# Kernel optimization log

Measured on AMD Instinct MI355X. Metric: run time of the kernel, lower is better.

The kernel has to match this reference:

```python
import jax, jax.numpy as jnp
import numpy as np

B, H, S, D = 65536, 512, 256, 64  # batch, hidden_dim, memory_slots, slot_size


def setup_inputs() -> dict:
    key = jax.random.key(0)
    ks = jax.random.split(key, 8)
    scale = 1.0 / np.sqrt(H)
    return {
        "query": jax.random.normal(ks[0], (B, H), jnp.float32),
        "content": jax.random.normal(ks[1], (B, H), jnp.float32),
        "memory": jax.random.normal(ks[2], (S, D), jnp.float32),
        "memory_age": jax.random.uniform(ks[3], (S,), jnp.float32, 0.0, 30.0),
        "W_read": jax.random.normal(ks[4], (H, S), jnp.float32) * scale,
        "b_read": jnp.zeros((S,), jnp.float32),
        "W_write": jax.random.normal(ks[5], (H, S), jnp.float32) * scale,
        "b_write": jnp.zeros((S,), jnp.float32),
        "W_content": jax.random.normal(ks[6], (H, D), jnp.float32) * scale,
        "b_content": jnp.zeros((D,), jnp.float32),
    }


def reference(query, content, memory, memory_age,
              W_read, b_read, W_write, b_write, W_content, b_content):
    # ---- read: attention-based addressing over memory slots ----
    read_weights = jax.nn.softmax(query @ W_read + b_read, axis=-1)      # [B, S]
    read_content = read_weights @ memory                                  # [B, D]

    # ---- write: consolidation dynamics (vectorized per-slot EMA) ----
    write_weights = jax.nn.softmax(query @ W_write + b_write, axis=-1)   # [B, S]
    processed_content = content @ W_content + b_content                   # [B, D]
    w_mean = write_weights.mean(axis=0)                                    # [S]
    c_mean = processed_content.mean(axis=0)                                # [D]

    active = w_mean > 0.01                                                 # [S] bool
    consolidation = jax.nn.sigmoid(memory_age * 0.1)                       # [S]
    # effective blend factor; zero for inactive slots (slot left untouched)
    alpha = jnp.where(active, w_mean * consolidation, 0.0)[:, None]        # [S, 1]
    new_memory = (1.0 - alpha) * memory + alpha * c_mean[None, :]          # [S, D]
    new_age = memory_age + active.astype(memory_age.dtype)                 # [S]

    return read_content, new_memory, new_age
```

## Files before the change

kernel.cpp:

```cpp
#include <hip/hip_runtime.h>


typedef short short8 __attribute__((ext_vector_type(8)));
typedef float floatx4 __attribute__((ext_vector_type(4)));

#define H_DIM 512
#define BM 32
#define BK 32

#define WS_WT    0
#define WS_MEMT  589824
#define WS_BFULL 622592
#define WS_WSUM  624896
#define WS_CSUM  625920

__device__ __forceinline__ unsigned short f2b(float f) {
  unsigned u = __float_as_uint(f);
  u += 0x7fffu + ((u >> 16) & 1u);
  return (unsigned short)(u >> 16);
}
__device__ __forceinline__ float b2f(unsigned short h) {
  return __uint_as_float(((unsigned)h) << 16);
}

__global__ void drcn_init(const float* __restrict__ W_read, const float* __restrict__ W_write,
                          const float* __restrict__ W_content, const float* __restrict__ b_read,
                          const float* __restrict__ b_write, const float* __restrict__ b_content,
                          const float* __restrict__ memory,
                          unsigned short* __restrict__ Wt, unsigned short* __restrict__ memT,
                          float* __restrict__ bfull, float* __restrict__ w_sum,
                          float* __restrict__ c_sum) {
  int idx = blockIdx.x * 256 + threadIdx.x;
  if (idx < 294912) {
    int n = idx >> 9, k = idx & 511;
    float v;
    if (n < 256)      v = W_read[k * 256 + n];
    else if (n < 512) v = W_write[k * 256 + (n - 256)];
    else              v = W_content[k * 64 + (n - 512)];
    Wt[idx] = f2b(v);
  } else if (idx < 311296) {
    int i = idx - 294912;
    int d = i >> 8, s = i & 255;
    memT[i] = f2b(memory[s * 64 + d]);
  } else if (idx < 311872) {
    int n = idx - 311296;
    bfull[n] = (n < 256) ? b_read[n] : (n < 512 ? b_write[n - 256] : b_content[n - 512]);
  } else if (idx < 312192) {
    int i = idx - 311872;
    if (i < 256) w_sum[i] = 0.0f; else c_sum[i - 256] = 0.0f;
  }
}

__global__ __launch_bounds__(256, 2) void drcn_main(
    const float* __restrict__ query, const float* __restrict__ content,
    const unsigned short* __restrict__ Wt, const float* __restrict__ bfull,
    const unsigned short* __restrict__ memT, float* __restrict__ w_sum,
    float* __restrict__ c_sum, float* __restrict__ out) {
  __shared__ __align__(16) char smem[51200];
  unsigned short* wt = (unsigned short*)smem;
  unsigned short* qa = (unsigned short*)(smem + 46080);
  unsigned short* ca = (unsigned short*)(smem + 48640);
  unsigned short* lg = (unsigned short*)smem;
  float* cs = (float*)(smem + 37376);
  float* cp = (float*)(smem + 38400);

  const int t = threadIdx.x;
  const int wv = t >> 6;
  const int ln = t & 63;
  const int ln15 = ln & 15;
  const int quad = ln >> 4;
  const int m0 = blockIdx.x * BM;

  float bias[9];
  #pragma unroll
  for (int j = 0; j < 9; j++) bias[j] = bfull[(wv * 9 + j) * 16 + ln15];

  floatx4 acc[2][9];
  #pragma unroll
  for (int mt = 0; mt < 2; mt++)
    #pragma unroll
    for (int j = 0; j < 9; j++) {
      floatx4 z = {0.0f, 0.0f, 0.0f, 0.0f};
      acc[mt][j] = z;
    }

  for (int k0 = 0; k0 < H_DIM; k0 += BK) {
    __syncthreads();
    #pragma unroll
    for (int j = 0; j < 9; j++) {
      int id = j * 256 + t;
      int n = id >> 2, q = id & 3;
      uint4 v = *(const uint4*)(Wt + n * 512 + k0 + q * 8);
      *(uint4*)(wt + n * 40 + q * 8) = v;
    }
    {
      int m = t >> 3, q = t & 7;
      const float4 fq = *(const float4*)(query + (size_t)(m0 + m) * H_DIM + k0 + q * 4);
      unsigned lo = (unsigned)f2b(fq.x) | ((unsigned)f2b(fq.y) << 16);
      unsigned hi = (unsigned)f2b(fq.z) | ((unsigned)f2b(fq.w) << 16);
      *(uint2*)(qa + m * 40 + q * 4) = make_uint2(lo, hi);
      const float4 fc = *(const float4*)(content + (size_t)(m0 + m) * H_DIM + k0 + q * 4);
      lo = (unsigned)f2b(fc.x) | ((unsigned)f2b(fc.y) << 16);
      hi = (unsigned)f2b(fc.z) | ((unsigned)f2b(fc.w) << 16);
      *(uint2*)(ca + m * 40 + q * 4) = make_uint2(lo, hi);
    }
    __syncthreads();

    short8 aq[2], ac[2];
    #pragma unroll
    for (int mt = 0; mt < 2; mt++) {
      aq[mt] = *(const short8*)(qa + (mt * 16 + ln15) * 40 + quad * 8);
      ac[mt] = *(const short8*)(ca + (mt * 16 + ln15) * 40 + quad * 8);
    }
    #pragma unroll
    for (int j = 0; j < 9; j++) {
      int nt = wv * 9 + j;
      short8 b = *(const short8*)(wt + (nt * 16 + ln15) * 40 + quad * 8);
      #pragma unroll
      for (int mt = 0; mt < 2; mt++) {
        short8 a = (nt >= 32) ? ac[mt] : aq[mt];
        acc[mt][j] = __builtin_amdgcn_mfma_f32_16x16x32_bf16(a, b, acc[mt][j], 0, 0, 0);
      }
    }
  }
  __syncthreads();

  #pragma unroll
  for (int j = 0; j < 9; j++) {
    int n = (wv * 9 + j) * 16 + ln15;
    #pragma unroll
    for (int mt = 0; mt < 2; mt++) {
      #pragma unroll
      for (int r = 0; r < 4; r++) {
        int row = mt * 16 + quad * 4 + r;
        lg[row * 584 + n] = f2b(acc[mt][j][r] + bias[j]);
      }
    }
  }
  cs[t] = 0.0f;
  if (t < 64) cp[t] = 0.0f;
  __syncthreads();

  const int r = t >> 3, c = t & 7;
  unsigned short* lrow = lg + r * 584;

  {
    float v[32];
    #pragma unroll
    for (int ch = 0; ch < 4; ch++) {
      short8 u = *(const short8*)(lrow + c * 32 + ch * 8);
      #pragma unroll
      for (int e = 0; e < 8; e++) v[ch * 8 + e] = b2f((unsigned short)u[e]);
    }
    float mx = -3.0e38f;
    #pragma unroll
    for (int i = 0; i < 32; i++) mx = fmaxf(mx, v[i]);
    mx = fmaxf(mx, __shfl_xor(mx, 1));
    mx = fmaxf(mx, __shfl_xor(mx, 2));
    mx = fmaxf(mx, __shfl_xor(mx, 4));
    float sm = 0.0f;
    #pragma unroll
    for (int i = 0; i < 32; i++) { v[i] = __expf(v[i] - mx); sm += v[i]; }
    sm += __shfl_xor(sm, 1);
    sm += __shfl_xor(sm, 2);
    sm += __shfl_xor(sm, 4);
    float inv = 1.0f / sm;
    #pragma unroll
    for (int ch = 0; ch < 4; ch++) {
      short8 u;
      #pragma unroll
      for (int e = 0; e < 8; e++) u[e] = (short)f2b(v[ch * 8 + e] * inv);
      *(short8*)(lrow + c * 32 + ch * 8) = u;
    }
  }
  {
    float v[32];
    #pragma unroll
    for (int ch = 0; ch < 4; ch++) {
      short8 u = *(const short8*)(lrow + 256 + c * 32 + ch * 8);
      #pragma unroll
      for (int e = 0; e < 8; e++) v[ch * 8 + e] = b2f((unsigned short)u[e]);
    }
    float mx = -3.0e38f;
    #pragma unroll
    for (int i = 0; i < 32; i++) mx = fmaxf(mx, v[i]);
    mx = fmaxf(mx, __shfl_xor(mx, 1));
    mx = fmaxf(mx, __shfl_xor(mx, 2));
    mx = fmaxf(mx, __shfl_xor(mx, 4));
    float sm = 0.0f;
    #pragma unroll
    for (int i = 0; i < 32; i++) { v[i] = __expf(v[i] - mx); sm += v[i]; }
    sm += __shfl_xor(sm, 1);
    sm += __shfl_xor(sm, 2);
    sm += __shfl_xor(sm, 4);
    float inv = 1.0f / sm;
    #pragma unroll
    for (int i = 0; i < 32; i++) {
      float p = v[i] * inv;
      p += __shfl_xor(p, 8);
      p += __shfl_xor(p, 16);
      p += __shfl_xor(p, 32);
      v[i] = p;
    }
    if (ln < 8) {
      #pragma unroll
      for (int i = 0; i < 32; i++) atomicAdd(&cs[c * 32 + i], v[i]);
    }
  }
  {
    float v[8];
    short8 u = *(const short8*)(lrow + 512 + c * 8);
    #pragma unroll
    for (int e = 0; e < 8; e++) v[e] = b2f((unsigned short)u[e]);
    #pragma unroll
    for (int e = 0; e < 8; e++) {
      float p = v[e];
      p += __shfl_xor(p, 8);
      p += __shfl_xor(p, 16);
      p += __shfl_xor(p, 32);
      v[e] = p;
    }
    if (ln < 8) {
      #pragma unroll
      for (int e = 0; e < 8; e++) atomicAdd(&cp[c * 8 + e], v[e]);
    }
  }
  __syncthreads();

  {
    int mt = wv & 1, nd0 = (wv >> 1) * 2;
    floatx4 ra[2];
    floatx4 z = {0.0f, 0.0f, 0.0f, 0.0f};
    ra[0] = z; ra[1] = z;
    #pragma unroll
    for (int ks = 0; ks < 8; ks++) {
      int s0 = ks * 32 + quad * 8;
      short8 a = *(const short8*)(lg + (mt * 16 + ln15) * 584 + s0);
      #pragma unroll
      for (int dt = 0; dt < 2; dt++) {
        short8 b = *(const short8*)(memT + ((nd0 + dt) * 16 + ln15) * 256 + s0);
        ra[dt] = __builtin_amdgcn_mfma_f32_16x16x32_bf16(a, b, ra[dt], 0, 0, 0);
      }
    }
    #pragma unroll
    for (int dt = 0; dt < 2; dt++)
      #pragma unroll
      for (int rr = 0; rr < 4; rr++) {
        int orow = m0 + mt * 16 + quad * 4 + rr;
        out[(size_t)orow * 64 + (nd0 + dt) * 16 + ln15] = ra[dt][rr];
      }
  }

  atomicAdd(&w_sum[t], cs[t]);
  if (t < 64) atomicAdd(&c_sum[t], cp[t]);
}

__global__ void drcn_final(const float* __restrict__ memory, const float* __restrict__ age,
                           const float* __restrict__ w_sum, const float* __restrict__ c_sum,
                           float* __restrict__ out_mem, float* __restrict__ out_age) {
  int idx = blockIdx.x * 256 + threadIdx.x;
  int s = idx >> 6, d = idx & 63;
  float wm = w_sum[s] * (1.0f / 65536.0f);
  bool act = wm > 0.01f;
  float cons = 1.0f / (1.0f + __expf(-age[s] * 0.1f));
  float alpha = act ? wm * cons : 0.0f;
  float cm = c_sum[d] * (1.0f / 65536.0f);
  out_mem[idx] = (1.0f - alpha) * memory[idx] + alpha * cm;
  if (d == 0) out_age[s] = age[s] + (act ? 1.0f : 0.0f);
}

extern "C" void kernel_launch(void* const* d_in, const int* in_sizes, int n_in,
                              void* d_out, int out_size, void* d_ws, size_t ws_size,
                              hipStream_t stream) {
  (void)in_sizes; (void)n_in; (void)out_size; (void)ws_size;
  const float* query     = (const float*)d_in[0];
  const float* content   = (const float*)d_in[1];
  const float* memory    = (const float*)d_in[2];
  const float* mem_age   = (const float*)d_in[3];
  const float* W_read    = (const float*)d_in[4];
  const float* b_read    = (const float*)d_in[5];
  const float* W_write   = (const float*)d_in[6];
  const float* b_write   = (const float*)d_in[7];
  const float* W_content = (const float*)d_in[8];
  const float* b_content = (const float*)d_in[9];
  float* out = (float*)d_out;
  char* ws = (char*)d_ws;
  unsigned short* Wt   = (unsigned short*)(ws + WS_WT);
  unsigned short* memT = (unsigned short*)(ws + WS_MEMT);
  float* bfull = (float*)(ws + WS_BFULL);
  float* w_sum = (float*)(ws + WS_WSUM);
  float* c_sum = (float*)(ws + WS_CSUM);

  drcn_init<<<1220, 256, 0, stream>>>(W_read, W_write, W_content, b_read, b_write,
                                      b_content, memory, Wt, memT, bfull, w_sum, c_sum);
  drcn_main<<<2048, 256, 0, stream>>>(query, content, Wt, bfull, memT, w_sum, c_sum, out);
  drcn_final<<<64, 256, 0, stream>>>(memory, mem_age, w_sum, c_sum,
                                     out + 4194304, out + 4210688);
}
```

Baseline: 494.9 us.

## Double-buffer weight tiles with async global-to-LDS loads and register-prefetch activations

The K-loop of the fused GEMM changes to a software pipeline. Each wave loads its own weight slab directly into a double-buffered LDS region with global_load_lds, and prefetches the next query/content fragments into registers. Activations are now converted to bf16 in registers and fed straight to the MFMA without an LDS round-trip, which removes both per-iteration __syncthreads. LDS use grows to 72KB per block, which may limit occupancy under launch_bounds(256,2). Correctness also relies on per-wave ownership of LDS and on vmcnt waits rather than barriers.

New measurement: 442.1 us. 10.7% less time.

```diff
diff --git a/kernel.cpp b/kernel.cpp
--- a/kernel.cpp
+++ b/kernel.cpp
@@ -1,4 +1,5 @@
 #include <hip/hip_runtime.h>
+#include <hip/hip_bf16.h>
 
 
 typedef short short8 __attribute__((ext_vector_type(8)));
@@ -6,7 +7,6 @@
 
 #define H_DIM 512
 #define BM 32
-#define BK 32
 
 #define WS_WT    0
 #define WS_MEMT  589824
@@ -21,6 +21,16 @@
 }
 __device__ __forceinline__ float b2f(unsigned short h) {
   return __uint_as_float(((unsigned)h) << 16);
+}
+__device__ __forceinline__ unsigned cvt2(float x, float y) {
+  union { __hip_bfloat162 h; unsigned u; } c;
+  c.h = __float22bfloat162_rn(make_float2(x, y));
+  return c.u;
+}
+__device__ __forceinline__ void async16(const void* g, void* l) {
+  __builtin_amdgcn_global_load_lds(
+      (const __attribute__((address_space(1))) unsigned int*)g,
+      (__attribute__((address_space(3))) unsigned int*)l, 16, 0, 0);
 }
 
 __global__ void drcn_init(const float* __restrict__ W_read, const float* __restrict__ W_write,
@@ -56,10 +66,7 @@
     const unsigned short* __restrict__ Wt, const float* __restrict__ bfull,
     const unsigned short* __restrict__ memT, float* __restrict__ w_sum,
     float* __restrict__ c_sum, float* __restrict__ out) {
-  __shared__ __align__(16) char smem[51200];
-  unsigned short* wt = (unsigned short*)smem;
-  unsigned short* qa = (unsigned short*)(smem + 46080);
-  unsigned short* ca = (unsigned short*)(smem + 48640);
+  __shared__ __align__(16) char smem[73728];
   unsigned short* lg = (unsigned short*)smem;
   float* cs = (float*)(smem + 37376);
   float* cp = (float*)(smem + 38400);
@@ -71,6 +78,17 @@
   const int quad = ln >> 4;
   const int m0 = blockIdx.x * BM;
 
+  const char* wsrc = (const char*)Wt +
+      (size_t)(((wv * 144 + (ln >> 2)) * 512 + (ln & 3) * 8) * 2);
+  char* wbase = smem + wv * 9216;
+
+  const float* qb[2]; const float* cb[2];
+  #pragma unroll
+  for (int mt = 0; mt < 2; mt++) {
+    qb[mt] = query   + (size_t)(m0 + mt * 16 + ln15) * H_DIM + quad * 8;
+    cb[mt] = content + (size_t)(m0 + mt * 16 + ln15) * H_DIM + quad * 8;
+  }
+
   float bias[9];
   #pragma unroll
   for (int j = 0; j < 9; j++) bias[j] = bfull[(wv * 9 + j) * 16 + ln15];
@@ -84,38 +102,57 @@
       acc[mt][j] = z;
     }
 
-  for (int k0 = 0; k0 < H_DIM; k0 += BK) {
-    __syncthreads();
+  float4 pq[2][2], pc[2][2];
+  #pragma unroll
+  for (int mt = 0; mt < 2; mt++) {
+    pq[mt][0] = *(const float4*)(qb[mt]);
+    pq[mt][1] = *(const float4*)(qb[mt] + 4);
+    pc[mt][0] = *(const float4*)(cb[mt]);
+    pc[mt][1] = *(const float4*)(cb[mt] + 4);
+  }
+  #pragma unroll
+  for (int j = 0; j < 9; j++)
+    async16(wsrc + j * 16384, wbase + j * 1024);
+
+  #pragma unroll 2
+  for (int it = 0; it < 16; ++it) {
+    short8 aq[2], ac[2];
+    #pragma unroll
+    for (int mt = 0; mt < 2; mt++) {
+      unsigned* p = (unsigned*)&aq[mt];
+      p[0] = cvt2(pq[mt][0].x, pq[mt][0].y);
+      p[1] = cvt2(pq[mt][0].z, pq[mt][0].w);
+      p[2] = cvt2(pq[mt][1].x, pq[mt][1].y);
+      p[3] = cvt2(pq[mt][1].z, pq[mt][1].w);
+      unsigned* q = (unsigned*)&ac[mt];
+      q[0] = cvt2(pc[mt][0].x, pc[mt][0].y);
+      q[1] = cvt2(pc[mt][0].z, pc[mt][0].w);
+      q[2] = cvt2(pc[mt][1].x, pc[mt][1].y);
+      q[3] = cvt2(pc[mt][1].z, pc[mt][1].w);
+    }
+    asm volatile("s_waitcnt vmcnt(0)" ::: "memory");
+
+    if (it < 15) {
+      const int k1 = (it + 1) * 32;
+      #pragma unroll
+      for (int mt = 0; mt < 2; mt++) {
+        pq[mt][0] = *(const float4*)(qb[mt] + k1);
+        pq[mt][1] = *(const float4*)(qb[mt] + k1 + 4);
+        pc[mt][0] = *(const float4*)(cb[mt] + k1);
+        pc[mt][1] = *(const float4*)(cb[mt] + k1 + 4);
+      }
+      const char* ws2 = wsrc + (size_t)(it + 1) * 64;
+      char* wd = smem + ((it + 1) & 1) * 36864 + wv * 9216;
+      #pragma unroll
+      for (int j = 0; j < 9; j++)
+        async16(ws2 + j * 16384, wd + j * 1024);
+    }
+
+    const char* rb = smem + (it & 1) * 36864 + wv * 9216;
     #pragma unroll
     for (int j = 0; j < 9; j++) {
-      int id = j * 256 + t;
-      int n = id >> 2, q = id & 3;
-      uint4 v = *(const uint4*)(Wt + n * 512 + k0 + q * 8);
-      *(uint4*)(wt + n * 40 + q * 8) = v;
-    }
-    {
-      int m = t >> 3, q = t & 7;
-      const float4 fq = *(const float4*)(query + (size_t)(m0 + m) * H_DIM + k0 + q * 4);
-      unsigned lo = (unsigned)f2b(fq.x) | ((unsigned)f2b(fq.y) << 16);
-      unsigned hi = (unsigned)f2b(fq.z) | ((unsigned)f2b(fq.w) << 16);
-      *(uint2*)(qa + m * 40 + q * 4) = make_uint2(lo, hi);
-      const float4 fc = *(const float4*)(content + (size_t)(m0 + m) * H_DIM + k0 + q * 4);
-      lo = (unsigned)f2b(fc.x) | ((unsigned)f2b(fc.y) << 16);
-      hi = (unsigned)f2b(fc.z) | ((unsigned)f2b(fc.w) << 16);
-      *(uint2*)(ca + m * 40 + q * 4) = make_uint2(lo, hi);
-    }
-    __syncthreads();
-
-    short8 aq[2], ac[2];
-    #pragma unroll
-    for (int mt = 0; mt < 2; mt++) {
-      aq[mt] = *(const short8*)(qa + (mt * 16 + ln15) * 40 + quad * 8);
-      ac[mt] = *(const short8*)(ca + (mt * 16 + ln15) * 40 + quad * 8);
-    }
-    #pragma unroll
-    for (int j = 0; j < 9; j++) {
-      int nt = wv * 9 + j;
-      short8 b = *(const short8*)(wt + (nt * 16 + ln15) * 40 + quad * 8);
+      short8 b = *(const short8*)(rb + j * 1024 + ln15 * 64 + quad * 16);
+      const int nt = wv * 9 + j;
       #pragma unroll
       for (int mt = 0; mt < 2; mt++) {
         short8 a = (nt >= 32) ? ac[mt] : aq[mt];
```

## Reorder content projection to project column mean, keep softmax in registers

Applied to the files above, without the earlier changes.

Uses linearity to drop the per-row content @ W_content GEMM. A separate kernel sums the content rows, and the final kernel projects that mean through W_content. The main kernel now computes only the 512 read/write logits, with softmax done in registers via cross-wave max/sum exchange through small LDS arrays. The write-weight column sum is reduced straight from registers with atomics. W tiles are loaded with async global-to-LDS copies, LDS shrinks, and occupancy rises to 4 blocks, at the cost of an extra kernel that reads content in fp32 and a changed summation order.

Measured after the change: 546.3 us. +10.4%, slower.

```diff
diff --git a/kernel.cpp b/kernel.cpp
--- a/kernel.cpp
+++ b/kernel.cpp
@@ -1,245 +1,246 @@
 #include <hip/hip_runtime.h>
+#include <hip/hip_bf16.h>
 
 
 typedef short short8 __attribute__((ext_vector_type(8)));
 typedef float floatx4 __attribute__((ext_vector_type(4)));
 
-#define H_DIM 512
-#define BM 32
-#define BK 32
-
 #define WS_WT    0
-#define WS_MEMT  589824
-#define WS_BFULL 622592
-#define WS_WSUM  624896
-#define WS_CSUM  625920
+#define WS_MEMT  524288
+#define WS_BFULL 557056
+#define WS_WSUM  559104
+#define WS_CMH   560128
 
 __device__ __forceinline__ unsigned short f2b(float f) {
   unsigned u = __float_as_uint(f);
   u += 0x7fffu + ((u >> 16) & 1u);
   return (unsigned short)(u >> 16);
 }
-__device__ __forceinline__ float b2f(unsigned short h) {
-  return __uint_as_float(((unsigned)h) << 16);
+__device__ __forceinline__ unsigned cvt2(float x, float y) {
+  union { __hip_bfloat162 h; unsigned u; } c;
+  c.h = __float22bfloat162_rn(make_float2(x, y));
+  return c.u;
+}
+__device__ __forceinline__ void async16(const void* g, void* l) {
+  __builtin_amdgcn_global_load_lds(
+      (const __attribute__((address_space(1))) unsigned int*)g,
+      (__attribute__((address_space(3))) unsigned int*)l, 16, 0, 0);
 }
 
 __global__ void drcn_init(const float* __restrict__ W_read, const float* __restrict__ W_write,
-                          const float* __restrict__ W_content, const float* __restrict__ b_read,
-                          const float* __restrict__ b_write, const float* __restrict__ b_content,
+                          const float* __restrict__ b_read, const float* __restrict__ b_write,
                           const float* __restrict__ memory,
                           unsigned short* __restrict__ Wt, unsigned short* __restrict__ memT,
                           float* __restrict__ bfull, float* __restrict__ w_sum,
-                          float* __restrict__ c_sum) {
+                          float* __restrict__ cmH) {
   int idx = blockIdx.x * 256 + threadIdx.x;
-  if (idx < 294912) {
+  if (idx < 262144) {
     int n = idx >> 9, k = idx & 511;
-    float v;
-    if (n < 256)      v = W_read[k * 256 + n];
-    else if (n < 512) v = W_write[k * 256 + (n - 256)];
-    else              v = W_content[k * 64 + (n - 512)];
+    float v = (n < 256) ? W_read[k * 256 + n] : W_write[k * 256 + (n - 256)];
     Wt[idx] = f2b(v);
-  } else if (idx < 311296) {
-    int i = idx - 294912;
+  } else if (idx < 278528) {
+    int i = idx - 262144;
     int d = i >> 8, s = i & 255;
     memT[i] = f2b(memory[s * 64 + d]);
-  } else if (idx < 311872) {
-    int n = idx - 311296;
-    bfull[n] = (n < 256) ? b_read[n] : (n < 512 ? b_write[n - 256] : b_content[n - 512]);
-  } else if (idx < 312192) {
-    int i = idx - 311872;
-    if (i < 256) w_sum[i] = 0.0f; else c_sum[i - 256] = 0.0f;
-  }
-}
-
-__global__ __launch_bounds__(256, 2) void drcn_main(
-    const float* __restrict__ query, const float* __restrict__ content,
-    const unsigned short* __restrict__ Wt, const float* __restrict__ bfull,
-    const unsigned short* __restrict__ memT, float* __restrict__ w_sum,
-    float* __restrict__ c_sum, float* __restrict__ out) {
-  __shared__ __align__(16) char smem[51200];
+  } else if (idx < 279040) {
+    int n = idx - 278528;
+    bfull[n] = (n < 256) ? b_read[n] : b_write[n - 256];
+  } else if (idx < 279296) {
+    w_sum[idx - 279040] = 0.0f;
+  } else if (idx < 279808) {
+    cmH[idx - 279296] = 0.0f;
+  }
+}
+
+__global__ __launch_bounds__(256) void drcn_cmean(const float* __restrict__ content,
+                                                  float* __restrict__ cmH) {
+  __shared__ float4 red[256];
+  const int t = threadIdx.x;
+  const int chunk = t & 127, rg = t >> 7;
+  const float4* src = (const float4*)content +
+      (size_t)(blockIdx.x * 32 + rg * 16) * 128 + chunk;
+  float4 s = {0.f, 0.f, 0.f, 0.f};
+  #pragma unroll
+  for (int i = 0; i < 16; i++) {
+    float4 v = src[(size_t)i * 128];
+    s.x += v.x; s.y += v.y; s.z += v.z; s.w += v.w;
+  }
+  red[t] = s;
+  __syncthreads();
+  if (t < 128) {
+    float4 a = red[t], b = red[t + 128];
+    atomicAdd(&cmH[t * 4 + 0], a.x + b.x);
+    atomicAdd(&cmH[t * 4 + 1], a.y + b.y);
+    atomicAdd(&cmH[t * 4 + 2], a.z + b.z);
+    atomicAdd(&cmH[t * 4 + 3], a.w + b.w);
+  }
+}
+
+__global__ __launch_bounds__(256, 4) void drcn_main(
+    const float* __restrict__ query, const unsigned short* __restrict__ Wt,
+    const float* __restrict__ bfull, const unsigned short* __restrict__ memT,
+    float* __restrict__ w_sum, float* __restrict__ out) {
+  __shared__ __align__(16) char smem[34816];
   unsigned short* wt = (unsigned short*)smem;
-  unsigned short* qa = (unsigned short*)(smem + 46080);
-  unsigned short* ca = (unsigned short*)(smem + 48640);
-  unsigned short* lg = (unsigned short*)smem;
-  float* cs = (float*)(smem + 37376);
-  float* cp = (float*)(smem + 38400);
+  unsigned short* qa = (unsigned short*)(smem + 32768);
+  unsigned short* pbuf = (unsigned short*)smem;
+  float* pmx  = (float*)(smem + 32768);
+  float* psum = (float*)(smem + 33280);
 
   const int t = threadIdx.x;
-  const int wv = t >> 6;
-  const int ln = t & 63;
-  const int ln15 = ln & 15;
-  const int quad = ln >> 4;
-  const int m0 = blockIdx.x * BM;
-
-  float bias[9];
-  #pragma unroll
-  for (int j = 0; j < 9; j++) bias[j] = bfull[(wv * 9 + j) * 16 + ln15];
-
-  floatx4 acc[2][9];
-  #pragma unroll
-  for (int mt = 0; mt < 2; mt++)
-    #pragma unroll
-    for (int j = 0; j < 9; j++) {
-      floatx4 z = {0.0f, 0.0f, 0.0f, 0.0f};
+  const int wv = t >> 6, ln = t & 63, ln15 = ln & 15, quad = ln >> 4;
+  const int m0 = blockIdx.x * 32;
+
+  float bias[8];
+  #pragma unroll
+  for (int j = 0; j < 8; j++) bias[j] = bfull[wv * 128 + j * 16 + ln15];
+
+  floatx4 acc[2][8];
+  #pragma unroll
+  for (int mt = 0; mt < 2; mt++)
+    #pragma unroll
+    for (int j = 0; j < 8; j++) {
+      floatx4 z = {0.f, 0.f, 0.f, 0.f};
       acc[mt][j] = z;
     }
 
-  for (int k0 = 0; k0 < H_DIM; k0 += BK) {
+  const unsigned short* wsrc = Wt + (size_t)(wv * 128 + (ln >> 2)) * 512 + (ln & 3) * 8;
+  char* wdst = smem + (wv * 8) * 1024 + ln * 16;
+  const int arow = t >> 3, acol = (t & 7) * 4;
+  const float* qsrc = query + (size_t)(m0 + arow) * 512 + acol;
+
+  for (int it = 0; it < 16; ++it) {
     __syncthreads();
     #pragma unroll
-    for (int j = 0; j < 9; j++) {
-      int id = j * 256 + t;
-      int n = id >> 2, q = id & 3;
-      uint4 v = *(const uint4*)(Wt + n * 512 + k0 + q * 8);
-      *(uint4*)(wt + n * 40 + q * 8) = v;
-    }
+    for (int i = 0; i < 8; i++)
+      async16(wsrc + (size_t)i * 16 * 512 + it * 32, wdst + i * 1024);
     {
-      int m = t >> 3, q = t & 7;
-      const float4 fq = *(const float4*)(query + (size_t)(m0 + m) * H_DIM + k0 + q * 4);
-      unsigned lo = (unsigned)f2b(fq.x) | ((unsigned)f2b(fq.y) << 16);
-      unsigned hi = (unsigned)f2b(fq.z) | ((unsigned)f2b(fq.w) << 16);
-      *(uint2*)(qa + m * 40 + q * 4) = make_uint2(lo, hi);
-      const float4 fc = *(const float4*)(content + (size_t)(m0 + m) * H_DIM + k0 + q * 4);
-      lo = (unsigned)f2b(fc.x) | ((unsigned)f2b(fc.y) << 16);
-      hi = (unsigned)f2b(fc.z) | ((unsigned)f2b(fc.w) << 16);
-      *(uint2*)(ca + m * 40 + q * 4) = make_uint2(lo, hi);
+      float4 f = *(const float4*)(qsrc + it * 32);
+      *(uint2*)(qa + arow * 32 + acol) = make_uint2(cvt2(f.x, f.y), cvt2(f.z, f.w));
     }
     __syncthreads();
 
-    short8 aq[2], ac[2];
-    #pragma unroll
-    for (int mt = 0; mt < 2; mt++) {
-      aq[mt] = *(const short8*)(qa + (mt * 16 + ln15) * 40 + quad * 8);
-      ac[mt] = *(const short8*)(ca + (mt * 16 + ln15) * 40 + quad * 8);
-    }
-    #pragma unroll
-    for (int j = 0; j < 9; j++) {
-      int nt = wv * 9 + j;
-      short8 b = *(const short8*)(wt + (nt * 16 + ln15) * 40 + quad * 8);
-      #pragma unroll
-      for (int mt = 0; mt < 2; mt++) {
-        short8 a = (nt >= 32) ? ac[mt] : aq[mt];
-        acc[mt][j] = __builtin_amdgcn_mfma_f32_16x16x32_bf16(a, b, acc[mt][j], 0, 0, 0);
+    short8 aq0 = *(const short8*)(qa + ln15 * 32 + quad * 8);
+    short8 aq1 = *(const short8*)(qa + (16 + ln15) * 32 + quad * 8);
+    #pragma unroll
+    for (int j = 0; j < 8; j++) {
+      short8 b = *(const short8*)(wt + (wv * 128 + j * 16 + ln15) * 32 + quad * 8);
+      acc[0][j] = __builtin_amdgcn_mfma_f32_16x16x32_bf16(aq0, b, acc[0][j], 0, 0, 0);
+      acc[1][j] = __builtin_amdgcn_mfma_f32_16x16x32_bf16(aq1, b, acc[1][j], 0, 0, 0);
+    }
+  }
+
+  #pragma unroll
+  for (int mt = 0; mt < 2; mt++)
+    #pragma unroll
+    for (int j = 0; j < 8; j++)
+      #pragma unroll
+      for (int r = 0; r < 4; r++) acc[mt][j][r] += bias[j];
+
+  float rmx[2][4];
+  #pragma unroll
+  for (int mt = 0; mt < 2; mt++)
+    #pragma unroll
+    for (int r = 0; r < 4; r++) {
+      float m = -3.0e38f;
+      #pragma unroll
+      for (int j = 0; j < 8; j++) m = fmaxf(m, acc[mt][j][r]);
+      rmx[mt][r] = m;
+    }
+  #pragma unroll
+  for (int b = 1; b <= 8; b <<= 1)
+    #pragma unroll
+    for (int mt = 0; mt < 2; mt++)
+      #pragma unroll
+      for (int r = 0; r < 4; r++) rmx[mt][r] = fmaxf(rmx[mt][r], __shfl_xor(rmx[mt][r], b));
+  if (ln15 == 0) {
+    #pragma unroll
+    for (int mt = 0; mt < 2; mt++)
+      #pragma unroll
+      for (int r = 0; r < 4; r++) pmx[wv * 32 + mt * 16 + quad * 4 + r] = rmx[mt][r];
+  }
+  __syncthreads();
+
+  float cmx[2][4], rsm[2][4];
+  #pragma unroll
+  for (int mt = 0; mt < 2; mt++)
+    #pragma unroll
+    for (int r = 0; r < 4; r++) {
+      int row = mt * 16 + quad * 4 + r;
+      cmx[mt][r] = fmaxf(pmx[wv * 32 + row], pmx[(wv ^ 1) * 32 + row]);
+      rsm[mt][r] = 0.f;
+    }
+  #pragma unroll
+  for (int mt = 0; mt < 2; mt++)
+    #pragma unroll
+    for (int j = 0; j < 8; j++)
+      #pragma unroll
+      for (int r = 0; r < 4; r++) {
+        float e = __expf(acc[mt][j][r] - cmx[mt][r]);
+        acc[mt][j][r] = e;
+        rsm[mt][r] += e;
       }
-    }
-  }
-  __syncthreads();
-
-  #pragma unroll
-  for (int j = 0; j < 9; j++) {
-    int n = (wv * 9 + j) * 16 + ln15;
-    #pragma unroll
-    for (int mt = 0; mt < 2; mt++) {
-      #pragma unroll
-      for (int r = 0; r < 4; r++) {
-        int row = mt * 16 + quad * 4 + r;
-        lg[row * 584 + n] = f2b(acc[mt][j][r] + bias[j]);
-      }
-    }
-  }
-  cs[t] = 0.0f;
-  if (t < 64) cp[t] = 0.0f;
-  __syncthreads();
-
-  const int r = t >> 3, c = t & 7;
-  unsigned short* lrow = lg + r * 584;
+  #pragma unroll
+  for (int b = 1; b <= 8; b <<= 1)
+    #pragma unroll
+    for (int mt = 0; mt < 2; mt++)
+      #pragma unroll
+      for (int r = 0; r < 4; r++) rsm[mt][r] += __shfl_xor(rsm[mt][r], b);
+  if (ln15 == 0) {
+    #pragma unroll
+    for (int mt = 0; mt < 2; mt++)
+      #pragma unroll
+      for (int r = 0; r < 4; r++) psum[wv * 32 + mt * 16 + quad * 4 + r] = rsm[mt][r];
+  }
+  __syncthreads();
+
+  float inv_[2][4];
+  #pragma unroll
+  for (int mt = 0; mt < 2; mt++)
+    #pragma unroll
+    for (int r = 0; r < 4; r++) {
+      int row = mt * 16 + quad * 4 + r;
+      inv_[mt][r] = 1.0f / (psum[wv * 32 + row] + psum[(wv ^ 1) * 32 + row]);
+    }
+
+  if (wv < 2) {
+    #pragma unroll
+    for (int mt = 0; mt < 2; mt++)
+      #pragma unroll
+      for (int j = 0; j < 8; j++)
+        #pragma unroll
+        for (int r = 0; r < 4; r++) {
+          int row = mt * 16 + quad * 4 + r;
+          pbuf[row * 264 + wv * 128 + j * 16 + ln15] = f2b(acc[mt][j][r] * inv_[mt][r]);
+        }
+  } else {
+    #pragma unroll
+    for (int j = 0; j < 8; j++) {
+      float s = 0.f;
+      #pragma unroll
+      for (int mt = 0; mt < 2; mt++)
+        #pragma unroll
+        for (int r = 0; r < 4; r++) s += acc[mt][j][r] * inv_[mt][r];
+      s += __shfl_xor(s, 16);
+      s += __shfl_xor(s, 32);
+      if (quad == 0) atomicAdd(&w_sum[(wv - 2) * 128 + j * 16 + ln15], s);
+    }
+  }
+  __syncthreads();
 
   {
-    float v[32];
-    #pragma unroll
-    for (int ch = 0; ch < 4; ch++) {
-      short8 u = *(const short8*)(lrow + c * 32 + ch * 8);
-      #pragma unroll
-      for (int e = 0; e < 8; e++) v[ch * 8 + e] = b2f((unsigned short)u[e]);
-    }
-    float mx = -3.0e38f;
-    #pragma unroll
-    for (int i = 0; i < 32; i++) mx = fmaxf(mx, v[i]);
-    mx = fmaxf(mx, __shfl_xor(mx, 1));
-    mx = fmaxf(mx, __shfl_xor(mx, 2));
-    mx = fmaxf(mx, __shfl_xor(mx, 4));
-    float sm = 0.0f;
-    #pragma unroll
-    for (int i = 0; i < 32; i++) { v[i] = __expf(v[i] - mx); sm += v[i]; }
-    sm += __shfl_xor(sm, 1);
-    sm += __shfl_xor(sm, 2);
-    sm += __shfl_xor(sm, 4);
-    float inv = 1.0f / sm;
-    #pragma unroll
-    for (int ch = 0; ch < 4; ch++) {
-      short8 u;
-      #pragma unroll
-      for (int e = 0; e < 8; e++) u[e] = (short)f2b(v[ch * 8 + e] * inv);
-      *(short8*)(lrow + c * 32 + ch * 8) = u;
-    }
-  }
-  {
-    float v[32];
-    #pragma unroll
-    for (int ch = 0; ch < 4; ch++) {
-      short8 u = *(const short8*)(lrow + 256 + c * 32 + ch * 8);
-      #pragma unroll
-      for (int e = 0; e < 8; e++) v[ch * 8 + e] = b2f((unsigned short)u[e]);
-    }
-    float mx = -3.0e38f;
-    #pragma unroll
-    for (int i = 0; i < 32; i++) mx = fmaxf(mx, v[i]);
-    mx = fmaxf(mx, __shfl_xor(mx, 1));
-    mx = fmaxf(mx, __shfl_xor(mx, 2));
-    mx = fmaxf(mx, __shfl_xor(mx, 4));
-    float sm = 0.0f;
-    #pragma unroll
-    for (int i = 0; i < 32; i++) { v[i] = __expf(v[i] - mx); sm += v[i]; }
-    sm += __shfl_xor(sm, 1);
-    sm += __shfl_xor(sm, 2);
-    sm += __shfl_xor(sm, 4);
-    float inv = 1.0f / sm;
-    #pragma unroll
-    for (int i = 0; i < 32; i++) {
-      float p = v[i] * inv;
-      p += __shfl_xor(p, 8);
-      p += __shfl_xor(p, 16);
-      p += __shfl_xor(p, 32);
-      v[i] = p;
-    }
-    if (ln < 8) {
-      #pragma unroll
-      for (int i = 0; i < 32; i++) atomicAdd(&cs[c * 32 + i], v[i]);
-    }
-  }
-  {
-    float v[8];
-    short8 u = *(const short8*)(lrow + 512 + c * 8);
-    #pragma unroll
-    for (int e = 0; e < 8; e++) v[e] = b2f((unsigned short)u[e]);
-    #pragma unroll
-    for (int e = 0; e < 8; e++) {
-      float p = v[e];
-      p += __shfl_xor(p, 8);
-      p += __shfl_xor(p, 16);
-      p += __shfl_xor(p, 32);
-      v[e] = p;
-    }
-    if (ln < 8) {
-      #pragma unroll
-      for (int e = 0; e < 8; e++) atomicAdd(&cp[c * 8 + e], v[e]);
-    }
-  }
-  __syncthreads();
-
-  {
-    int mt = wv & 1, nd0 = (wv >> 1) * 2;
+    const int mt = wv & 1, dn0 = (wv >> 1) * 2;
     floatx4 ra[2];
-    floatx4 z = {0.0f, 0.0f, 0.0f, 0.0f};
+    floatx4 z = {0.f, 0.f, 0.f, 0.f};
     ra[0] = z; ra[1] = z;
     #pragma unroll
     for (int ks = 0; ks < 8; ks++) {
       int s0 = ks * 32 + quad * 8;
-      short8 a = *(const short8*)(lg + (mt * 16 + ln15) * 584 + s0);
+      short8 a = *(const short8*)(pbuf + (mt * 16 + ln15) * 264 + s0);
       #pragma unroll
       for (int dt = 0; dt < 2; dt++) {
-        short8 b = *(const short8*)(memT + ((nd0 + dt) * 16 + ln15) * 256 + s0);
-        ra[dt] = __builtin_amdgcn_mfma_f32_16x16x32_bf16(a, b, ra[dt], 0, 0, 0);
+        short8 bb = *(const short8*)(memT + ((dn0 + dt) * 16 + ln15) * 256 + s0);
+        ra[dt] = __builtin_amdgcn_mfma_f32_16x16x32_bf16(a, bb, ra[dt], 0, 0, 0);
       }
     }
     #pragma unroll
@@ -247,26 +248,38 @@
       #pragma unroll
       for (int rr = 0; rr < 4; rr++) {
         int orow = m0 + mt * 16 + quad * 4 + rr;
-        out[(size_t)orow * 64 + (nd0 + dt) * 16 + ln15] = ra[dt][rr];
+        out[(size_t)orow * 64 + (dn0 + dt) * 16 + ln15] = ra[dt][rr];
       }
   }
-
-  atomicAdd(&w_sum[t], cs[t]);
-  if (t < 64) atomicAdd(&c_sum[t], cp[t]);
-}
-
-__global__ void drcn_final(const float* __restrict__ memory, const float* __restrict__ age,
-                           const float* __restrict__ w_sum, const float* __restrict__ c_sum,
-                           float* __restrict__ out_mem, float* __restrict__ out_age) {
-  int idx = blockIdx.x * 256 + threadIdx.x;
-  int s = idx >> 6, d = idx & 63;
-  float wm = w_sum[s] * (1.0f / 65536.0f);
+}
+
+__global__ __launch_bounds__(256) void drcn_final(
+    const float* __restrict__ memory, const float* __restrict__ age,
+    const float* __restrict__ w_sum, const float* __restrict__ cmH,
+    const float* __restrict__ W_content, const float* __restrict__ b_content,
+    float* __restrict__ out_mem, float* __restrict__ out_age) {
+  __shared__ float part[4][64];
+  __shared__ float pc[64];
+  const int t = threadIdx.x;
+  {
+    int d = t & 63, p = t >> 6;
+    float s = 0.f;
+    for (int h = p * 128; h < p * 128 + 128; h++) s += cmH[h] * W_content[h * 64 + d];
+    part[p][d] = s;
+  }
+  __syncthreads();
+  if (t < 64)
+    pc[t] = b_content[t] +
+            (part[0][t] + part[1][t] + part[2][t] + part[3][t]) * (1.0f / 65536.0f);
+  __syncthreads();
+  int idx = blockIdx.x * 256 + t;
+  int s_ = idx >> 6, d = idx & 63;
+  float wm = w_sum[s_] * (1.0f / 65536.0f);
   bool act = wm > 0.01f;
-  float cons = 1.0f / (1.0f + __expf(-age[s] * 0.1f));
+  float cons = 1.0f / (1.0f + __expf(-age[s_] * 0.1f));
   float alpha = act ? wm * cons : 0.0f;
-  float cm = c_sum[d] * (1.0f / 65536.0f);
-  out_mem[idx] = (1.0f - alpha) * memory[idx] + alpha * cm;
-  if (d == 0) out_age[s] = age[s] + (act ? 1.0f : 0.0f);
+  out_mem[idx] = (1.0f - alpha) * memory[idx] + alpha * pc[d];
+  if (d == 0) out_age[s_] = age[s_] + (act ? 1.0f : 0.0f);
 }
 
 extern "C" void kernel_launch(void* const* d_in, const int* in_sizes, int n_in,
@@ -289,11 +302,12 @@
   unsigned short* memT = (unsigned short*)(ws + WS_MEMT);
   float* bfull = (float*)(ws + WS_BFULL);
   float* w_sum = (float*)(ws + WS_WSUM);
-  float* c_sum = (float*)(ws + WS_CSUM);
-
-  drcn_init<<<1220, 256, 0, stream>>>(W_read, W_write, W_content, b_read, b_write,
-                                      b_content, memory, Wt, memT, bfull, w_sum, c_sum);
-  drcn_main<<<2048, 256, 0, stream>>>(query, content, Wt, bfull, memT, w_sum, c_sum, out);
-  drcn_final<<<64, 256, 0, stream>>>(memory, mem_age, w_sum, c_sum,
-                                     out + 4194304, out + 4210688);
-}
+  float* cmH   = (float*)(ws + WS_CMH);
+
+  drcn_init<<<1093, 256, 0, stream>>>(W_read, W_write, b_read, b_write, memory,
+                                      Wt, memT, bfull, w_sum, cmH);
+  drcn_cmean<<<2048, 256, 0, stream>>>(content, cmH);
+  drcn_main<<<2048, 256, 0, stream>>>(query, Wt, bfull, memT, w_sum, out);
+  drcn_final<<<64, 256, 0, stream>>>(memory, mem_age, w_sum, cmH, W_content,
+                                     b_content, out + 4194304, out + 4210688);
+}
```
